# Optimization experiments

Hardware: AMD Instinct MI355X
Metric: run time of the kernel (lower is better)

Reference implementation:

```python
import jax, jax.numpy as jnp
import numpy as np

EMBED_DIM = 1024
NUM_HEADS = 16
HEAD_DIM = EMBED_DIM // NUM_HEADS


def setup_inputs() -> dict:
    key = jax.random.key(0)
    ks = jax.random.split(key, 9)
    B, S, D = 4, 2048, EMBED_DIM
    s = 1.0 / np.sqrt(D)
    return {
        "x": jax.random.normal(ks[0], (B, S, D), dtype=jnp.float32),
        "Wq": jax.random.uniform(ks[1], (D, D), jnp.float32, -s, s),
        "bq": jax.random.uniform(ks[2], (D,), jnp.float32, -s, s),
        "Wk": jax.random.uniform(ks[3], (D, D), jnp.float32, -s, s),
        "bk": jax.random.uniform(ks[4], (D,), jnp.float32, -s, s),
        "Wv": jax.random.uniform(ks[5], (D, D), jnp.float32, -s, s),
        "bv": jax.random.uniform(ks[6], (D,), jnp.float32, -s, s),
        "Wo": jax.random.uniform(ks[7], (D, D), jnp.float32, -s, s),
        "bo": jax.random.uniform(ks[8], (D,), jnp.float32, -s, s),
    }


def reference(x, Wq, bq, Wk, bk, Wv, bv, Wo, bo):
    B, S, D = x.shape
    H, Hd = NUM_HEADS, HEAD_DIM

    def proj(W, b):
        # torch Linear: x @ W.T + b; reshape to [B, H, S, Hd]
        y = jnp.einsum('bsd,ed->bse', x, W) + b
        return y.reshape(B, S, H, Hd).transpose(0, 2, 1, 3)

    Q = proj(Wq, bq)
    K = proj(Wk, bk)
    V = proj(Wv, bv)
    scores = jnp.einsum('bhqd,bhkd->bhqk', Q, K) / np.sqrt(Hd).astype(jnp.float32)
    attn = jax.nn.softmax(scores, axis=-1)
    out = jnp.einsum('bhqk,bhkd->bhqd', attn, V)
    out = out.transpose(0, 2, 1, 3).reshape(B, S, D)
    return jnp.einsum('bsd,ed->bse', out, Wo) + bo
```

## Files before the change

kernel.cpp:

```cpp
#include <hip/hip_runtime.h>
#include <stdint.h>

typedef unsigned short u16;
typedef _Float16 f16;
typedef __fp16 fp16x2 __attribute__((ext_vector_type(2)));
typedef f16 f16x8 __attribute__((ext_vector_type(8)));
typedef float f32x4 __attribute__((ext_vector_type(4)));
typedef u16 u16x8v __attribute__((ext_vector_type(8)));

#define MFMAH __builtin_amdgcn_mfma_f32_16x16x32_f16

__device__ __forceinline__ void gload16(const void* g, void* l) {
    __builtin_amdgcn_global_load_lds(
        (const __attribute__((address_space(1))) uint32_t*)g,
        (__attribute__((address_space(3))) uint32_t*)l, 16, 0, 0);
}

__global__ __launch_bounds__(256) void convert_x(const float4* __restrict__ x,
                                                 f16x8* __restrict__ o) {
    int i = blockIdx.x * 256 + threadIdx.x;
    float4 a = x[2 * i], b = x[2 * i + 1];
    f16x8 h;
    h[0] = (f16)a.x; h[1] = (f16)a.y; h[2] = (f16)a.z; h[3] = (f16)a.w;
    h[4] = (f16)b.x; h[5] = (f16)b.y; h[6] = (f16)b.z; h[7] = (f16)b.w;
    o[i] = h;
}

__global__ __launch_bounds__(256) void convert_w(const float4* __restrict__ Wq,
                                                 const float4* __restrict__ Wk,
                                                 const float4* __restrict__ Wv,
                                                 const float4* __restrict__ Wo,
                                                 f16x8* __restrict__ hi,
                                                 f16x8* __restrict__ lo) {
    int gi = blockIdx.x * 256 + threadIdx.x;
    int wsel = gi >> 17;
    int li = gi & 131071;
    const float4* src = (wsel == 0) ? Wq : (wsel == 1) ? Wk : (wsel == 2) ? Wv : Wo;
    float4 a = src[2 * li], b = src[2 * li + 1];
    float v[8] = {a.x, a.y, a.z, a.w, b.x, b.y, b.z, b.w};
    f16x8 h, l;
#pragma unroll
    for (int j = 0; j < 8; ++j) {
        h[j] = (f16)v[j];
        l[j] = (f16)(v[j] - (float)h[j]);
    }
    hi[gi] = h; lo[gi] = l;
}

template <bool QKV>
__global__ __launch_bounds__(256, 2)
void gemm_wsplit(const f16* __restrict__ A,
                 const f16* __restrict__ Whi, const f16* __restrict__ Wlo,
                 const float* __restrict__ b0, const float* __restrict__ b1,
                 const float* __restrict__ b2,
                 f16* __restrict__ oq, f16* __restrict__ ok, f16* __restrict__ ov,
                 float* __restrict__ ofp) {
    __shared__ f16 ldsA[128 * 64];
    __shared__ f16 ldsW[2][128 * 64];
    const int t = threadIdx.x;
    const int lane = t & 63, quad = lane >> 4, l16 = lane & 15;
    const int wid = t >> 6;
    const int wsel = QKV ? (blockIdx.x >> 3) : 3;
    const int bm = blockIdx.y * 128;
    const int bn = (QKV ? (blockIdx.x & 7) : blockIdx.x) * 128;
    const int wm = (wid >> 1) * 64, wn = (wid & 1) * 64;
    const f16* Wh = Whi + (QKV ? (size_t)wsel * 1048576 : 0);
    const f16* Wl = Wlo + (QKV ? (size_t)wsel * 1048576 : 0);
    const float* bias = QKV ? ((wsel == 0) ? b0 : (wsel == 1) ? b1 : b2) : b0;

    f32x4 acc[4][4] = {};

    for (int kt = 0; kt < 16; ++kt) {
        __syncthreads();
        const int k0 = kt * 64;
#pragma unroll
        for (int c = 0; c < 4; ++c) {
            const int u = c * 256 + t;
            const int r = u >> 3, cc = u & 7;
            const int sc = cc ^ (r & 7);
            gload16(A + (size_t)(bm + r) * 1024 + k0 + sc * 8, &ldsA[u * 8]);
        }
#pragma unroll
        for (int p = 0; p < 2; ++p) {
            const f16* Ws = p ? Wl : Wh;
#pragma unroll
            for (int c = 0; c < 4; ++c) {
                const int u = c * 256 + t;
                const int r = u >> 3, cc = u & 7;
                const int sc = cc ^ (r & 7);
                gload16(Ws + (size_t)(bn + r) * 1024 + k0 + sc * 8, &ldsW[p][u * 8]);
            }
        }
        __syncthreads();

#pragma unroll
        for (int kq = 0; kq < 2; ++kq) {
            f16x8 af[4], bh[4], bl[4];
            const int chb = kq * 4 + quad;
#pragma unroll
            for (int i = 0; i < 4; ++i) {
                const int ra = wm + i * 16 + l16;
                const int ch = chb ^ (l16 & 7);
                af[i] = *(const f16x8*)&ldsA[ra * 64 + ch * 8];
                const int rb = wn + i * 16 + l16;
                bh[i] = *(const f16x8*)&ldsW[0][rb * 64 + ch * 8];
                bl[i] = *(const f16x8*)&ldsW[1][rb * 64 + ch * 8];
            }
#pragma unroll
            for (int mi = 0; mi < 4; ++mi)
#pragma unroll
                for (int ni = 0; ni < 4; ++ni) {
                    acc[mi][ni] = MFMAH(af[mi], bh[ni], acc[mi][ni], 0, 0, 0);
                    acc[mi][ni] = MFMAH(af[mi], bl[ni], acc[mi][ni], 0, 0, 0);
                }
        }
    }

#pragma unroll
    for (int ni = 0; ni < 4; ++ni) {
        const int e = bn + wn + ni * 16 + l16;
        const float bv = bias[e];
#pragma unroll
        for (int mi = 0; mi < 4; ++mi) {
            const int row0 = bm + wm + mi * 16 + quad * 4;
            if (!QKV) {
#pragma unroll
                for (int r = 0; r < 4; ++r)
                    ofp[(size_t)(row0 + r) * 1024 + e] = acc[mi][ni][r] + bv;
            } else if (wsel == 2) {
                const int b = row0 >> 11, s0 = row0 & 2047;
                const int h = e >> 6, d = e & 63;
                ushort4 pk;
                f16 p0 = (f16)(acc[mi][ni][0] + bv);
                f16 p1 = (f16)(acc[mi][ni][1] + bv);
                f16 p2 = (f16)(acc[mi][ni][2] + bv);
                f16 p3 = (f16)(acc[mi][ni][3] + bv);
                pk.x = __builtin_bit_cast(u16, p0);
                pk.y = __builtin_bit_cast(u16, p1);
                pk.z = __builtin_bit_cast(u16, p2);
                pk.w = __builtin_bit_cast(u16, p3);
                *(ushort4*)(ov + ((size_t)((b * 16 + h) * 64 + d)) * 2048 + s0) = pk;
            } else {
                const int h = e >> 6, d = e & 63;
                f16* dst = (wsel == 0) ? oq : ok;
#pragma unroll
                for (int r = 0; r < 4; ++r) {
                    const int row = row0 + r;
                    const int b = row >> 11, s = row & 2047;
                    float v = acc[mi][ni][r] + bv;
                    if (wsel == 0) v *= 0.18033688f;
                    dst[((size_t)((b * 16 + h) * 2048 + s)) * 64 + d] = (f16)v;
                }
            }
        }
    }
}

__global__ __launch_bounds__(256, 2)
void attn_fused(const f16* __restrict__ Q, const f16* __restrict__ K,
                const f16* __restrict__ Vt, f16* __restrict__ AO) {
    __shared__ f16 Kt[128 * 64];
    __shared__ f16 Vs[64 * 128];
    __shared__ __align__(16) f16 Pw[4][4][16 * 48];
    const int t = threadIdx.x, wid = t >> 6, lane = t & 63;
    const int quad = lane >> 4, l16 = lane & 15;
    const int sw7 = l16 & 7;
    const int bh = blockIdx.x;
    const int q0 = blockIdx.y * 256;
    const size_t base = (size_t)bh * (2048 * 64);

    const u16x8v ou = {0x3C00, 0x3C00, 0x3C00, 0x3C00, 0x3C00, 0x3C00, 0x3C00, 0x3C00};
    const f16x8 ONES = __builtin_bit_cast(f16x8, ou);

    f16x8 qf[4][2];
#pragma unroll
    for (int s = 0; s < 4; ++s) {
        const int qrow = q0 + wid * 64 + s * 16 + l16;
        qf[s][0] = *(const f16x8*)(Q + base + (size_t)qrow * 64 + quad * 8);
        qf[s][1] = *(const f16x8*)(Q + base + (size_t)qrow * 64 + 32 + quad * 8);
    }

    f32x4 of[4][4] = {};
    f32x4 rs[4] = {};

    for (int kt = 0; kt < 16; ++kt) {
        __syncthreads();
#pragma unroll
        for (int c = 0; c < 4; ++c) {
            const int u = c * 256 + t;
            const int row = u >> 3, cc = u & 7;
            const int sc = cc ^ (row & 7);
            gload16(K + base + (size_t)(kt * 128 + row) * 64 + sc * 8, &Kt[u * 8]);
        }
#pragma unroll
        for (int c = 0; c < 4; ++c) {
            const int u = c * 256 + t;
            const int row = u >> 4, cc = u & 15;
            const int sc = cc ^ (row & 15);
            gload16(Vt + base + (size_t)row * 2048 + kt * 128 + sc * 8, &Vs[u * 8]);
        }
        __syncthreads();

#pragma unroll
        for (int kk = 0; kk < 4; ++kk) {
#pragma unroll
            for (int nn = 0; nn < 2; ++nn) {
                const int row = (kk * 2 + nn) * 16 + l16;
                const f16x8 kb0 = *(const f16x8*)&Kt[row * 64 + (quad ^ sw7) * 8];
                const f16x8 kb1 = *(const f16x8*)&Kt[row * 64 + ((4 | quad) ^ sw7) * 8];
#pragma unroll
                for (int s = 0; s < 4; ++s) {
                    f32x4 sf = {};
                    sf = MFMAH(kb0, qf[s][0], sf, 0, 0, 0);
                    sf = MFMAH(kb1, qf[s][1], sf, 0, 0, 0);
                    const float p0 = __builtin_amdgcn_exp2f(sf[0]);
                    const float p1 = __builtin_amdgcn_exp2f(sf[1]);
                    const float p2 = __builtin_amdgcn_exp2f(sf[2]);
                    const float p3 = __builtin_amdgcn_exp2f(sf[3]);
                    const fp16x2 d0 = __builtin_amdgcn_cvt_pkrtz(p0, p1);
                    const fp16x2 d1 = __builtin_amdgcn_cvt_pkrtz(p2, p3);
                    uint2 pk;
                    pk.x = __builtin_bit_cast(uint32_t, d0);
                    pk.y = __builtin_bit_cast(uint32_t, d1);
                    *(uint2*)&Pw[wid][s][l16 * 48 + nn * 16 + quad * 4] = pk;
                }
            }
            f16x8 pf[4];
#pragma unroll
            for (int s = 0; s < 4; ++s)
                pf[s] = *(const f16x8*)&Pw[wid][s][l16 * 48 + quad * 8];
#pragma unroll
            for (int di = 0; di < 4; ++di) {
                const int row = di * 16 + l16;
                const f16x8 vb = *(const f16x8*)&Vs[row * 128 + ((kk * 4 + quad) ^ l16) * 8];
#pragma unroll
                for (int s = 0; s < 4; ++s)
                    of[s][di] = MFMAH(pf[s], vb, of[s][di], 0, 0, 0);
            }
#pragma unroll
            for (int s = 0; s < 4; ++s)
                rs[s] = MFMAH(pf[s], ONES, rs[s], 0, 0, 0);
        }
    }

    const int b = bh >> 4, h = bh & 15;
#pragma unroll
    for (int s = 0; s < 4; ++s)
#pragma unroll
        for (int di = 0; di < 4; ++di) {
            const int e = h * 64 + di * 16 + l16;
#pragma unroll
            for (int r = 0; r < 4; ++r) {
                const int srow = q0 + wid * 64 + s * 16 + quad * 4 + r;
                AO[(size_t)(b * 2048 + srow) * 1024 + e] = (f16)(of[s][di][r] / rs[s][r]);
            }
        }
}

extern "C" void kernel_launch(void* const* d_in, const int* in_sizes, int n_in,
                              void* d_out, int out_size, void* d_ws, size_t ws_size,
                              hipStream_t stream) {
    const float* x  = (const float*)d_in[0];
    const float* Wq = (const float*)d_in[1];
    const float* bq = (const float*)d_in[2];
    const float* Wk = (const float*)d_in[3];
    const float* bk = (const float*)d_in[4];
    const float* Wv = (const float*)d_in[5];
    const float* bv = (const float*)d_in[6];
    const float* Wo = (const float*)d_in[7];
    const float* bo = (const float*)d_in[8];
    float* out = (float*)d_out;

    char* ws = (char*)d_ws;
    f16* XF  = (f16*)(ws);
    f16* WH  = (f16*)(ws + (16u << 20));
    f16* WL  = (f16*)(ws + (24u << 20));
    f16* QF  = (f16*)(ws + (32u << 20));
    f16* KF  = (f16*)(ws + (48u << 20));
    f16* VTF = (f16*)(ws + (64u << 20));
    f16* AOF = (f16*)(ws + (80u << 20));

    convert_x<<<4096, 256, 0, stream>>>((const float4*)x, (f16x8*)XF);
    convert_w<<<2048, 256, 0, stream>>>((const float4*)Wq, (const float4*)Wk,
                                        (const float4*)Wv, (const float4*)Wo,
                                        (f16x8*)WH, (f16x8*)WL);

    gemm_wsplit<true><<<dim3(24, 64), 256, 0, stream>>>(
        XF, WH, WL, bq, bk, bv, QF, KF, VTF, nullptr);

    attn_fused<<<dim3(64, 8), 256, 0, stream>>>(QF, KF, VTF, AOF);

    gemm_wsplit<false><<<dim3(8, 64), 256, 0, stream>>>(
        AOF, WH + 3145728, WL + 3145728, bo, bo, bo, nullptr, nullptr, nullptr, out);
}
```

Baseline: 319.6 us.

## Split QKV/O GEMMs, enlarge QKV tile to 256 rows, transpose attention PV MFMA

The QKV projection GEMM becomes its own kernel with 512 threads and a 256x128 tile, so each W tile loaded into LDS is shared by twice as many rows. The output projection gets its own 256-thread kernel. In attention, the PV and rowsum MFMAs swap operands so each lane holds four consecutive head-dim values, which allows packed 8-byte stores to AO with one reciprocal per row instead of a divide per element. The P scratch row stride changes from 48 to 50 to reduce LDS bank conflicts, at the cost of splitting the 8-byte P writes into two 4-byte stores. A fragments are also loaded per mi to reduce register pressure. Risks include the higher LDS use and the occupancy hint of 4 blocks per CU for the larger QKV block.

```diff
diff --git a/kernel.cpp b/kernel.cpp
--- a/kernel.cpp
+++ b/kernel.cpp
@@ -47,26 +47,24 @@
     hi[gi] = h; lo[gi] = l;
 }
 
-template <bool QKV>
-__global__ __launch_bounds__(256, 2)
-void gemm_wsplit(const f16* __restrict__ A,
-                 const f16* __restrict__ Whi, const f16* __restrict__ Wlo,
-                 const float* __restrict__ b0, const float* __restrict__ b1,
-                 const float* __restrict__ b2,
-                 f16* __restrict__ oq, f16* __restrict__ ok, f16* __restrict__ ov,
-                 float* __restrict__ ofp) {
-    __shared__ f16 ldsA[128 * 64];
+__global__ __launch_bounds__(512, 4)
+void gemm_qkv(const f16* __restrict__ A,
+              const f16* __restrict__ Whi, const f16* __restrict__ Wlo,
+              const float* __restrict__ b0, const float* __restrict__ b1,
+              const float* __restrict__ b2,
+              f16* __restrict__ oq, f16* __restrict__ ok, f16* __restrict__ ov) {
+    __shared__ f16 ldsA[256 * 64];
     __shared__ f16 ldsW[2][128 * 64];
     const int t = threadIdx.x;
     const int lane = t & 63, quad = lane >> 4, l16 = lane & 15;
     const int wid = t >> 6;
-    const int wsel = QKV ? (blockIdx.x >> 3) : 3;
-    const int bm = blockIdx.y * 128;
-    const int bn = (QKV ? (blockIdx.x & 7) : blockIdx.x) * 128;
+    const int wsel = blockIdx.x >> 3;
+    const int bm = blockIdx.y * 256;
+    const int bn = (blockIdx.x & 7) * 128;
     const int wm = (wid >> 1) * 64, wn = (wid & 1) * 64;
-    const f16* Wh = Whi + (QKV ? (size_t)wsel * 1048576 : 0);
-    const f16* Wl = Wlo + (QKV ? (size_t)wsel * 1048576 : 0);
-    const float* bias = QKV ? ((wsel == 0) ? b0 : (wsel == 1) ? b1 : b2) : b0;
+    const f16* Wh = Whi + (size_t)wsel * 1048576;
+    const f16* Wl = Wlo + (size_t)wsel * 1048576;
+    const float* bias = (wsel == 0) ? b0 : (wsel == 1) ? b1 : b2;
 
     f32x4 acc[4][4] = {};
 
@@ -75,7 +73,7 @@
         const int k0 = kt * 64;
 #pragma unroll
         for (int c = 0; c < 4; ++c) {
-            const int u = c * 256 + t;
+            const int u = c * 512 + t;
             const int r = u >> 3, cc = u & 7;
             const int sc = cc ^ (r & 7);
             gload16(A + (size_t)(bm + r) * 1024 + k0 + sc * 8, &ldsA[u * 8]);
@@ -84,8 +82,8 @@
         for (int p = 0; p < 2; ++p) {
             const f16* Ws = p ? Wl : Wh;
 #pragma unroll
-            for (int c = 0; c < 4; ++c) {
-                const int u = c * 256 + t;
+            for (int c = 0; c < 2; ++c) {
+                const int u = c * 512 + t;
                 const int r = u >> 3, cc = u & 7;
                 const int sc = cc ^ (r & 7);
                 gload16(Ws + (size_t)(bn + r) * 1024 + k0 + sc * 8, &ldsW[p][u * 8]);
@@ -95,24 +93,25 @@
 
 #pragma unroll
         for (int kq = 0; kq < 2; ++kq) {
-            f16x8 af[4], bh[4], bl[4];
+            f16x8 bh[4], bl[4];
             const int chb = kq * 4 + quad;
+            const int ch = chb ^ (l16 & 7);
 #pragma unroll
             for (int i = 0; i < 4; ++i) {
-                const int ra = wm + i * 16 + l16;
-                const int ch = chb ^ (l16 & 7);
-                af[i] = *(const f16x8*)&ldsA[ra * 64 + ch * 8];
                 const int rb = wn + i * 16 + l16;
                 bh[i] = *(const f16x8*)&ldsW[0][rb * 64 + ch * 8];
                 bl[i] = *(const f16x8*)&ldsW[1][rb * 64 + ch * 8];
             }
 #pragma unroll
-            for (int mi = 0; mi < 4; ++mi)
+            for (int mi = 0; mi < 4; ++mi) {
+                const int ra = wm + mi * 16 + l16;
+                const f16x8 af = *(const f16x8*)&ldsA[ra * 64 + ch * 8];
 #pragma unroll
                 for (int ni = 0; ni < 4; ++ni) {
-                    acc[mi][ni] = MFMAH(af[mi], bh[ni], acc[mi][ni], 0, 0, 0);
-                    acc[mi][ni] = MFMAH(af[mi], bl[ni], acc[mi][ni], 0, 0, 0);
+                    acc[mi][ni] = MFMAH(af, bh[ni], acc[mi][ni], 0, 0, 0);
+                    acc[mi][ni] = MFMAH(af, bl[ni], acc[mi][ni], 0, 0, 0);
                 }
+            }
         }
     }
 
@@ -120,16 +119,12 @@
     for (int ni = 0; ni < 4; ++ni) {
         const int e = bn + wn + ni * 16 + l16;
         const float bv = bias[e];
+        const int h = e >> 6, d = e & 63;
 #pragma unroll
         for (int mi = 0; mi < 4; ++mi) {
             const int row0 = bm + wm + mi * 16 + quad * 4;
-            if (!QKV) {
-#pragma unroll
-                for (int r = 0; r < 4; ++r)
-                    ofp[(size_t)(row0 + r) * 1024 + e] = acc[mi][ni][r] + bv;
-            } else if (wsel == 2) {
+            if (wsel == 2) {
                 const int b = row0 >> 11, s0 = row0 & 2047;
-                const int h = e >> 6, d = e & 63;
                 ushort4 pk;
                 f16 p0 = (f16)(acc[mi][ni][0] + bv);
                 f16 p1 = (f16)(acc[mi][ni][1] + bv);
@@ -141,7 +136,6 @@
                 pk.w = __builtin_bit_cast(u16, p3);
                 *(ushort4*)(ov + ((size_t)((b * 16 + h) * 64 + d)) * 2048 + s0) = pk;
             } else {
-                const int h = e >> 6, d = e & 63;
                 f16* dst = (wsel == 0) ? oq : ok;
 #pragma unroll
                 for (int r = 0; r < 4; ++r) {
@@ -157,11 +151,85 @@
 }
 
 __global__ __launch_bounds__(256, 2)
+void gemm_o(const f16* __restrict__ A,
+            const f16* __restrict__ Wh, const f16* __restrict__ Wl,
+            const float* __restrict__ bias, float* __restrict__ ofp) {
+    __shared__ f16 ldsA[128 * 64];
+    __shared__ f16 ldsW[2][128 * 64];
+    const int t = threadIdx.x;
+    const int lane = t & 63, quad = lane >> 4, l16 = lane & 15;
+    const int wid = t >> 6;
+    const int bm = blockIdx.y * 128, bn = blockIdx.x * 128;
+    const int wm = (wid >> 1) * 64, wn = (wid & 1) * 64;
+
+    f32x4 acc[4][4] = {};
+
+    for (int kt = 0; kt < 16; ++kt) {
+        __syncthreads();
+        const int k0 = kt * 64;
+#pragma unroll
+        for (int c = 0; c < 4; ++c) {
+            const int u = c * 256 + t;
+            const int r = u >> 3, cc = u & 7;
+            const int sc = cc ^ (r & 7);
+            gload16(A + (size_t)(bm + r) * 1024 + k0 + sc * 8, &ldsA[u * 8]);
+        }
+#pragma unroll
+        for (int p = 0; p < 2; ++p) {
+            const f16* Ws = p ? Wl : Wh;
+#pragma unroll
+            for (int c = 0; c < 4; ++c) {
+                const int u = c * 256 + t;
+                const int r = u >> 3, cc = u & 7;
+                const int sc = cc ^ (r & 7);
+                gload16(Ws + (size_t)(bn + r) * 1024 + k0 + sc * 8, &ldsW[p][u * 8]);
+            }
+        }
+        __syncthreads();
+
+#pragma unroll
+        for (int kq = 0; kq < 2; ++kq) {
+            f16x8 bh[4], bl[4];
+            const int ch = (kq * 4 + quad) ^ (l16 & 7);
+#pragma unroll
+            for (int i = 0; i < 4; ++i) {
+                const int rb = wn + i * 16 + l16;
+                bh[i] = *(const f16x8*)&ldsW[0][rb * 64 + ch * 8];
+                bl[i] = *(const f16x8*)&ldsW[1][rb * 64 + ch * 8];
+            }
+#pragma unroll
+            for (int mi = 0; mi < 4; ++mi) {
+                const int ra = wm + mi * 16 + l16;
+                const f16x8 af = *(const f16x8*)&ldsA[ra * 64 + ch * 8];
+#pragma unroll
+                for (int ni = 0; ni < 4; ++ni) {
+                    acc[mi][ni] = MFMAH(af, bh[ni], acc[mi][ni], 0, 0, 0);
+                    acc[mi][ni] = MFMAH(af, bl[ni], acc[mi][ni], 0, 0, 0);
+                }
+            }
+        }
+    }
+
+#pragma unroll
+    for (int ni = 0; ni < 4; ++ni) {
+        const int e = bn + wn + ni * 16 + l16;
+        const float bv = bias[e];
+#pragma unroll
+        for (int mi = 0; mi < 4; ++mi) {
+            const int row0 = bm + wm + mi * 16 + quad * 4;
+#pragma unroll
+            for (int r = 0; r < 4; ++r)
+                ofp[(size_t)(row0 + r) * 1024 + e] = acc[mi][ni][r] + bv;
+        }
+    }
+}
+
+__global__ __launch_bounds__(256, 2)
 void attn_fused(const f16* __restrict__ Q, const f16* __restrict__ K,
                 const f16* __restrict__ Vt, f16* __restrict__ AO) {
     __shared__ f16 Kt[128 * 64];
     __shared__ f16 Vs[64 * 128];
-    __shared__ __align__(16) f16 Pw[4][4][16 * 48];
+    __shared__ f16 Pw[4][4][16 * 50];
     const int t = threadIdx.x, wid = t >> 6, lane = t & 63;
     const int quad = lane >> 4, l16 = lane & 15;
     const int sw7 = l16 & 7;
@@ -219,42 +287,49 @@
                     const float p3 = __builtin_amdgcn_exp2f(sf[3]);
                     const fp16x2 d0 = __builtin_amdgcn_cvt_pkrtz(p0, p1);
                     const fp16x2 d1 = __builtin_amdgcn_cvt_pkrtz(p2, p3);
-                    uint2 pk;
-                    pk.x = __builtin_bit_cast(uint32_t, d0);
-                    pk.y = __builtin_bit_cast(uint32_t, d1);
-                    *(uint2*)&Pw[wid][s][l16 * 48 + nn * 16 + quad * 4] = pk;
+                    uint32_t* pp = (uint32_t*)&Pw[wid][s][l16 * 50 + nn * 16 + quad * 4];
+                    pp[0] = __builtin_bit_cast(uint32_t, d0);
+                    pp[1] = __builtin_bit_cast(uint32_t, d1);
                 }
             }
             f16x8 pf[4];
 #pragma unroll
             for (int s = 0; s < 4; ++s)
-                pf[s] = *(const f16x8*)&Pw[wid][s][l16 * 48 + quad * 8];
+                pf[s] = *(const f16x8*)&Pw[wid][s][l16 * 50 + quad * 8];
 #pragma unroll
             for (int di = 0; di < 4; ++di) {
                 const int row = di * 16 + l16;
                 const f16x8 vb = *(const f16x8*)&Vs[row * 128 + ((kk * 4 + quad) ^ l16) * 8];
 #pragma unroll
                 for (int s = 0; s < 4; ++s)
-                    of[s][di] = MFMAH(pf[s], vb, of[s][di], 0, 0, 0);
+                    of[s][di] = MFMAH(vb, pf[s], of[s][di], 0, 0, 0);
             }
 #pragma unroll
             for (int s = 0; s < 4; ++s)
-                rs[s] = MFMAH(pf[s], ONES, rs[s], 0, 0, 0);
+                rs[s] = MFMAH(ONES, pf[s], rs[s], 0, 0, 0);
         }
     }
 
     const int b = bh >> 4, h = bh & 15;
 #pragma unroll
-    for (int s = 0; s < 4; ++s)
+    for (int s = 0; s < 4; ++s) {
+        const int qrow = q0 + wid * 64 + s * 16 + l16;
+        const float inv = 1.0f / rs[s][0];
 #pragma unroll
         for (int di = 0; di < 4; ++di) {
-            const int e = h * 64 + di * 16 + l16;
-#pragma unroll
-            for (int r = 0; r < 4; ++r) {
-                const int srow = q0 + wid * 64 + s * 16 + quad * 4 + r;
-                AO[(size_t)(b * 2048 + srow) * 1024 + e] = (f16)(of[s][di][r] / rs[s][r]);
-            }
-        }
+            const int e0 = h * 64 + di * 16 + quad * 4;
+            ushort4 pk;
+            f16 o0 = (f16)(of[s][di][0] * inv);
+            f16 o1 = (f16)(of[s][di][1] * inv);
+            f16 o2 = (f16)(of[s][di][2] * inv);
+            f16 o3 = (f16)(of[s][di][3] * inv);
+            pk.x = __builtin_bit_cast(u16, o0);
+            pk.y = __builtin_bit_cast(u16, o1);
+            pk.z = __builtin_bit_cast(u16, o2);
+            pk.w = __builtin_bit_cast(u16, o3);
+            *(ushort4*)(AO + (size_t)(b * 2048 + qrow) * 1024 + e0) = pk;
+        }
+    }
 }
 
 extern "C" void kernel_launch(void* const* d_in, const int* in_sizes, int n_in,
@@ -285,11 +360,9 @@
                                         (const float4*)Wv, (const float4*)Wo,
                                         (f16x8*)WH, (f16x8*)WL);
 
-    gemm_wsplit<true><<<dim3(24, 64), 256, 0, stream>>>(
-        XF, WH, WL, bq, bk, bv, QF, KF, VTF, nullptr);
+    gemm_qkv<<<dim3(24, 32), 512, 0, stream>>>(XF, WH, WL, bq, bk, bv, QF, KF, VTF);
 
     attn_fused<<<dim3(64, 8), 256, 0, stream>>>(QF, KF, VTF, AOF);
 
-    gemm_wsplit<false><<<dim3(8, 64), 256, 0, stream>>>(
-        AOF, WH + 3145728, WL + 3145728, bo, bo, bo, nullptr, nullptr, nullptr, out);
-}
+    gemm_o<<<dim3(8, 64), 256, 0, stream>>>(AOF, WH + 3145728, WL + 3145728, bo, out);
+}
```

Result: faster. 300.0 us (-6.1%).
